# Kernel tuning notes

Measured on AMD Instinct MI355X. Metric: run time of the kernel, lower is better.

## Reference

```python
import jax, jax.numpy as jnp
import numpy as np

N, E, D, HID, HEADS, G = 20000, 320000, 1280, 64, 4, 256
NEG_SLOPE = 0.2  # PyG GATv2Conv default negative_slope


def setup_inputs() -> dict:
    key = jax.random.key(0)
    ks = jax.random.split(key, 20)

    def w(k, shape, fan_in):
        return (jax.random.normal(k, shape, jnp.float32) / np.float32(np.sqrt(fan_in)))

    return {
        "x": jax.random.normal(ks[0], (N, D), jnp.float32),
        "edge_index": jax.random.randint(ks[1], (2, E), 0, N),
        "batch": jnp.sort(jax.random.randint(ks[2], (N,), 0, G)),
        # GATv2 layer 1: in D, out HID, heads HEADS, concat
        "Wl1": w(ks[3], (D, HEADS * HID), D),
        "bl1": w(ks[4], (HEADS * HID,), D),
        "Wr1": w(ks[5], (D, HEADS * HID), D),
        "br1": w(ks[6], (HEADS * HID,), D),
        "att1": w(ks[7], (HEADS, HID), HID),
        "bias1": jnp.zeros((HEADS * HID,), jnp.float32),
        # GATv2 layer 2: in HEADS*HID, out HID, heads 1, concat
        "Wl2": w(ks[8], (HEADS * HID, HID), HEADS * HID),
        "bl2": w(ks[9], (HID,), HEADS * HID),
        "Wr2": w(ks[10], (HEADS * HID, HID), HEADS * HID),
        "br2": w(ks[11], (HID,), HEADS * HID),
        "att2": w(ks[12], (1, HID), HID),
        "bias2": jnp.zeros((HID,), jnp.float32),
        # MLP head
        "W3": w(ks[13], (HID, HID), HID),
        "b3": w(ks[14], (HID,), HID),
        "W4": w(ks[15], (HID, 1), HID),
        "b4": w(ks[16], (1,), HID),
    }


def _gatv2(x, src, dst, Wl, bl, Wr, br, att, bias, n):
    """PyG GATv2Conv (concat=True, eval mode): e_ij = a^T LeakyReLU(Wl x_j + Wr x_i),
    per-destination softmax, out_i = sum_j alpha_ij * (Wl x_j)."""
    H, C = att.shape
    xl = (x @ Wl + bl).reshape(n, H, C)  # source transform
    xr = (x @ Wr + br).reshape(n, H, C)  # target transform
    e = jax.nn.leaky_relu(xl[src] + xr[dst], NEG_SLOPE)      # [E,H,C]
    logit = jnp.einsum('ehc,hc->eh', e, att)                  # [E,H]
    m = jax.ops.segment_max(logit, dst, num_segments=n)      # stable softmax per dst
    ex = jnp.exp(logit - m[dst])
    denom = jax.ops.segment_sum(ex, dst, num_segments=n)
    alpha = ex / (denom[dst] + 1e-16)                         # [E,H]
    out = jax.ops.segment_sum(xl[src] * alpha[:, :, None], dst, num_segments=n)
    return out.reshape(n, H * C) + bias


def reference(x, edge_index, batch, Wl1, bl1, Wr1, br1, att1, bias1,
              Wl2, bl2, Wr2, br2, att2, bias2, W3, b3, W4, b4):
    # add_self_loops=True (PyG default)
    loops = jnp.arange(N, dtype=edge_index.dtype)
    src = jnp.concatenate([edge_index[0], loops])
    dst = jnp.concatenate([edge_index[1], loops])
    h = jax.nn.relu(_gatv2(x, src, dst, Wl1, bl1, Wr1, br1, att1, bias1, N))
    h = jax.nn.relu(_gatv2(h, src, dst, Wl2, bl2, Wr2, br2, att2, bias2, N))
    g = jax.ops.segment_sum(h, batch, num_segments=G)  # global_add_pool -> [G,HID]
    return jax.nn.relu(g @ W3 + b3) @ W4 + b4          # [G,1]
```

## Files before the change

kernel.cpp:

```cpp
#include <hip/hip_runtime.h>

constexpr int Nn    = 20000;
constexpr int Ee    = 320000;
constexpr int Dd    = 1280;
constexpr int Gg    = 256;
constexpr int ETOT  = Ee + Nn;
#define NEG 0.2f

typedef __attribute__((ext_vector_type(8))) short s8v;
typedef __attribute__((ext_vector_type(8))) unsigned short u16x8;
typedef __attribute__((ext_vector_type(4))) float f4v;

__device__ inline float lrelu(float v){ return v > 0.f ? v : NEG * v; }
__device__ inline float wave_sum(float v){
  #pragma unroll
  for(int o = 32; o; o >>= 1) v += __shfl_xor(v, o, 64);
  return v;
}
__device__ inline unsigned short f2bf(float x){
  unsigned u = __float_as_uint(x);
  return (unsigned short)((u + 0x7FFFu + ((u >> 16) & 1u)) >> 16);
}
__device__ inline float bf2f(unsigned short h){ return __uint_as_float(((unsigned)h) << 16); }

__device__ inline void async_cp16(const void* g, void* l){
  __builtin_amdgcn_global_load_lds((const __attribute__((address_space(1))) void*)g,
                                   (__attribute__((address_space(3))) void*)l, 16, 0, 0);
}

__device__ inline size_t pkoff(int n, int k, int NITp){
  return ((((size_t)(n >> 7) * NITp + (k >> 5)) * 512)
          + (((k >> 3) & 3) * 128 + (n & 127))) * 8 + (k & 7);
}

__global__ void fill_int(int* p, int n, int v){
  int i = blockIdx.x * blockDim.x + threadIdx.x;
  if(i < n) p[i] = v;
}
__global__ void hist_dst(const int* __restrict__ dst, int* __restrict__ deg){
  int e = blockIdx.x * blockDim.x + threadIdx.x;
  if(e < Ee) atomicAdd(&deg[dst[e]], 1);
}
__global__ __launch_bounds__(1024) void scan_deg(const int* __restrict__ deg,
                                                 int* __restrict__ rowptr,
                                                 int* __restrict__ cursor){
  __shared__ int part[1024];
  int t = threadIdx.x;
  const int CH = (Nn + 1023) / 1024;
  int base = t * CH;
  int s = 0;
  for(int j = 0; j < CH; j++){ int idx = base + j; if(idx < Nn) s += deg[idx]; }
  part[t] = s;
  __syncthreads();
  for(int off = 1; off < 1024; off <<= 1){
    int v = (t >= off) ? part[t - off] : 0;
    __syncthreads();
    part[t] += v;
    __syncthreads();
  }
  int acc = part[t] - s;
  for(int j = 0; j < CH; j++){
    int idx = base + j;
    if(idx < Nn){ rowptr[idx] = acc; cursor[idx] = acc; acc += deg[idx]; }
  }
  if(t == 1023) rowptr[Nn] = part[1023];
}
__global__ void scatter_edges(const int* __restrict__ src, const int* __restrict__ dst,
                              int* __restrict__ cursor, int* __restrict__ srcv){
  int e = blockIdx.x * blockDim.x + threadIdx.x;
  if(e >= ETOT) return;
  int d, s;
  if(e < Ee){ d = dst[e]; s = src[e]; } else { d = e - Ee; s = d; }
  int pos = atomicAdd(&cursor[d], 1);
  srcv[pos] = s;
}

__global__ __launch_bounds__(256) void wsplit(const float* __restrict__ Wl,
                                              const float* __restrict__ Wr,
                                              int K, int Ca, int NITp,
                                              unsigned short* __restrict__ PBH,
                                              unsigned short* __restrict__ PBL){
  __shared__ float t[32][33];
  int k0 = blockIdx.x * 32, n0 = blockIdx.y * 32;
  int tx = threadIdx.x & 31, ty = threadIdx.x >> 5;
  #pragma unroll
  for(int j = 0; j < 4; j++){
    int kk = ty + j * 8;
    int n = n0 + tx;
    t[kk][tx] = (n < Ca) ? Wl[(size_t)(k0 + kk) * Ca + n]
                         : Wr[(size_t)(k0 + kk) * Ca + (n - Ca)];
  }
  __syncthreads();
  #pragma unroll
  for(int j = 0; j < 4; j++){
    int nn = ty + j * 8;
    float v = t[tx][nn];
    unsigned short hi = f2bf(v);
    unsigned short lo = f2bf(v - bf2f(hi));
    size_t o = pkoff(n0 + nn, k0 + tx, NITp);
    PBH[o] = hi;
    PBL[o] = lo;
  }
}

__global__ __launch_bounds__(512) void gemm_2t(
    const float* __restrict__ X, int K, int niter, int nty,
    const unsigned short* __restrict__ PBH, const unsigned short* __restrict__ PBL,
    const float* __restrict__ bl, const float* __restrict__ br,
    unsigned short* __restrict__ XLb, float* __restrict__ XR)
{
  int id = blockIdx.x;
  int g8 = id >> 5, rem = id & 31;
  int xb = rem >> 3, yb = g8 * 8 + (rem & 7);
  if(yb >= nty) return;

  __shared__ unsigned short sA [2][4096];
  __shared__ unsigned short sBh[2][4096];
  __shared__ unsigned short sBl[2][4096];

  const int tid  = threadIdx.x;
  const int lane = tid & 63;
  const int w    = tid >> 6;
  const int wm   = w & 1, wn = w >> 1;
  const int bm   = yb * 128;
  const int bn   = xb * 128;

  f4v acc[4][2] = {};

  const int ar = w * 16 + (lane >> 2);
  const int aq = lane & 3;
  int gmr = bm + ar; if(gmr >= Nn) gmr = Nn - 1;
  const float* aptr = X + (size_t)gmr * K + aq * 8;
  const int awoff = (aq * 128 + ((ar + aq * 4) & 127)) * 8;

  const size_t bbase = ((size_t)xb * niter) * 4096 + tid * 8;
  const unsigned short* bhp = PBH + bbase;
  const unsigned short* blp = PBL + bbase;
  const int bldsoff = w * 512;

  async_cp16(bhp, &sBh[0][bldsoff]);
  async_cp16(blp, &sBl[0][bldsoff]);
  {
    float4 v0 = *(const float4*)(aptr);
    float4 v1 = *(const float4*)(aptr + 4);
    float fv[8] = {v0.x, v0.y, v0.z, v0.w, v1.x, v1.y, v1.z, v1.w};
    u16x8 hv;
    #pragma unroll
    for(int q = 0; q < 8; q++) hv[q] = f2bf(fv[q]);
    *(u16x8*)&sA[0][awoff] = hv;
  }

  const int mr = lane & 15;
  const int gq = lane >> 4;
  int aoff[4], boff[2];
  #pragma unroll
  for(int i = 0; i < 4; i++){
    int row = wm * 64 + i * 16 + mr;
    aoff[i] = (gq * 128 + ((row + gq * 4) & 127)) * 8;
  }
  #pragma unroll
  for(int j = 0; j < 2; j++){
    int n = wn * 32 + j * 16 + mr;
    boff[j] = (gq * 128 + n) * 8;
  }

  for(int it = 0; it < niter; it++){
    const int cur = it & 1, nxt = cur ^ 1;
    __syncthreads();
    float4 v0, v1;
    const bool more = (it + 1 < niter);
    if(more){
      async_cp16(bhp + (size_t)(it + 1) * 4096, &sBh[nxt][bldsoff]);
      async_cp16(blp + (size_t)(it + 1) * 4096, &sBl[nxt][bldsoff]);
      v0 = *(const float4*)(aptr + (it + 1) * 32);
      v1 = *(const float4*)(aptr + (it + 1) * 32 + 4);
    }
    s8v ah[4];
    #pragma unroll
    for(int i = 0; i < 4; i++) ah[i] = *(const s8v*)&sA[cur][aoff[i]];
    #pragma unroll
    for(int j = 0; j < 2; j++){
      s8v bh  = *(const s8v*)&sBh[cur][boff[j]];
      s8v bl2 = *(const s8v*)&sBl[cur][boff[j]];
      #pragma unroll
      for(int i = 0; i < 4; i++){
        acc[i][j] = __builtin_amdgcn_mfma_f32_16x16x32_bf16(ah[i], bh,  acc[i][j], 0, 0, 0);
        acc[i][j] = __builtin_amdgcn_mfma_f32_16x16x32_bf16(ah[i], bl2, acc[i][j], 0, 0, 0);
      }
    }
    if(more){
      float fv[8] = {v0.x, v0.y, v0.z, v0.w, v1.x, v1.y, v1.z, v1.w};
      u16x8 hv;
      #pragma unroll
      for(int q = 0; q < 8; q++) hv[q] = f2bf(fv[q]);
      *(u16x8*)&sA[nxt][awoff] = hv;
    }
  }

  const int quad = lane >> 4, col = lane & 15;
  #pragma unroll
  for(int j = 0; j < 2; j++){
    int gn = bn + wn * 32 + j * 16 + col;
    #pragma unroll
    for(int i = 0; i < 4; i++){
      #pragma unroll
      for(int rg = 0; rg < 4; rg++){
        int gmm = bm + wm * 64 + i * 16 + quad * 4 + rg;
        if(gmm < Nn){
          float v = acc[i][j][rg];
          if(gn < 256) XLb[(size_t)gmm * 256 + gn] = f2bf(v + bl[gn]);
          else         XR [(size_t)gmm * 256 + (gn - 256)] = v + br[gn - 256];
        }
      }
    }
  }
}

__global__ __launch_bounds__(512) void gemm2_cp(
    const unsigned short* __restrict__ PA,
    const unsigned short* __restrict__ PBH, const unsigned short* __restrict__ PBL,
    const float* __restrict__ bl, const float* __restrict__ br,
    unsigned short* __restrict__ XLb, float* __restrict__ XR)
{
  const int yb = blockIdx.x;
  __shared__ unsigned short sA [2][2048];
  __shared__ unsigned short sBh[2][4096];
  __shared__ unsigned short sBl[2][4096];

  const int tid  = threadIdx.x;
  const int lane = tid & 63;
  const int w    = tid >> 6;
  const int wm   = w & 1, wn = w >> 1;
  const int bm   = yb * 64;
  const int NIT  = 8;

  f4v acc[2][2] = {};

  const unsigned short* bhp = PBH + tid * 8;
  const unsigned short* blp = PBL + tid * 8;
  const int bldsoff = w * 512;
  const unsigned short* pap = PA + ((size_t)yb * NIT * 256 + tid) * 8;
  const int aldsoff = w * 512;

  async_cp16(bhp, &sBh[0][bldsoff]);
  async_cp16(blp, &sBl[0][bldsoff]);
  if(w < 4) async_cp16(pap, &sA[0][aldsoff]);

  const int mr = lane & 15;
  const int gq = lane >> 4;
  int aoff[2], boff[2];
  #pragma unroll
  for(int i = 0; i < 2; i++) aoff[i] = (gq * 64 + wm * 32 + i * 16 + mr) * 8;
  #pragma unroll
  for(int j = 0; j < 2; j++) boff[j] = (gq * 128 + wn * 32 + j * 16 + mr) * 8;

  for(int it = 0; it < NIT; it++){
    const int cur = it & 1, nxt = cur ^ 1;
    __syncthreads();
    if(it + 1 < NIT){
      async_cp16(bhp + (size_t)(it + 1) * 4096, &sBh[nxt][bldsoff]);
      async_cp16(blp + (size_t)(it + 1) * 4096, &sBl[nxt][bldsoff]);
      if(w < 4) async_cp16(pap + (size_t)(it + 1) * 2048, &sA[nxt][aldsoff]);
    }
    s8v ah[2];
    #pragma unroll
    for(int i = 0; i < 2; i++) ah[i] = *(const s8v*)&sA[cur][aoff[i]];
    #pragma unroll
    for(int j = 0; j < 2; j++){
      s8v bh  = *(const s8v*)&sBh[cur][boff[j]];
      s8v bl2 = *(const s8v*)&sBl[cur][boff[j]];
      #pragma unroll
      for(int i = 0; i < 2; i++){
        acc[i][j] = __builtin_amdgcn_mfma_f32_16x16x32_bf16(ah[i], bh,  acc[i][j], 0, 0, 0);
        acc[i][j] = __builtin_amdgcn_mfma_f32_16x16x32_bf16(ah[i], bl2, acc[i][j], 0, 0, 0);
      }
    }
  }

  const int quad = lane >> 4, col = lane & 15;
  #pragma unroll
  for(int j = 0; j < 2; j++){
    int gn = wn * 32 + j * 16 + col;
    #pragma unroll
    for(int i = 0; i < 2; i++){
      #pragma unroll
      for(int rg = 0; rg < 4; rg++){
        int gmm = bm + wm * 32 + i * 16 + quad * 4 + rg;
        if(gmm < Nn){
          float v = acc[i][j][rg];
          if(gn < 64) XLb[(size_t)gmm * 64 + gn] = f2bf(v + bl[gn]);
          else        XR [(size_t)gmm * 64 + (gn - 64)] = v + br[gn - 64];
        }
      }
    }
  }
}

__global__ __launch_bounds__(256) void gat_fused1(
    const int* __restrict__ rowptr, const int* __restrict__ srcv,
    const unsigned short* __restrict__ XLb, const float* __restrict__ XR,
    const float* __restrict__ att, const float* __restrict__ bias,
    unsigned short* __restrict__ PA2)
{
  int node = blockIdx.x * 4 + (threadIdx.x >> 6);
  int lane = threadIdx.x & 63;
  if(node >= Nn) return;
  const float4 xr = *(const float4*)(XR + (size_t)node * 256 + lane * 4);
  const float4 a  = *(const float4*)(att + lane * 4);
  int r0 = rowptr[node], r1 = rowptr[node + 1];
  float m[4], l[4]; float4 acc[4];
  #pragma unroll
  for(int c = 0; c < 4; c++){ m[c] = -1e30f; l[c] = 0.f; acc[c] = make_float4(0,0,0,0); }
  for(int k = r0; k < r1; k += 4){
    int nv = r1 - k;
    int s[4]; float4 xl[4]; float p[4];
    #pragma unroll
    for(int c = 0; c < 4; c++){
      int kk = (c < nv) ? (k + c) : k;
      s[c] = srcv[kk];
    }
    #pragma unroll
    for(int c = 0; c < 4; c++){
      ushort4 u = *(const ushort4*)(XLb + (size_t)s[c] * 256 + lane * 4);
      xl[c] = make_float4(bf2f(u.x), bf2f(u.y), bf2f(u.z), bf2f(u.w));
    }
    #pragma unroll
    for(int c = 0; c < 4; c++){
      p[c] = lrelu(xl[c].x + xr.x) * a.x + lrelu(xl[c].y + xr.y) * a.y
           + lrelu(xl[c].z + xr.z) * a.z + lrelu(xl[c].w + xr.w) * a.w;
    }
    #pragma unroll
    for(int o = 8; o; o >>= 1){
      #pragma unroll
      for(int c = 0; c < 4; c++) p[c] += __shfl_xor(p[c], o, 64);
    }
    #pragma unroll
    for(int c = 0; c < 4; c++){
      if(c < nv){
        float mn = fmaxf(m[c], p[c]);
        float sc = __expf(m[c] - mn);
        float wg = __expf(p[c] - mn);
        l[c] = l[c] * sc + wg;
        acc[c].x = acc[c].x * sc + wg * xl[c].x;
        acc[c].y = acc[c].y * sc + wg * xl[c].y;
        acc[c].z = acc[c].z * sc + wg * xl[c].z;
        acc[c].w = acc[c].w * sc + wg * xl[c].w;
        m[c] = mn;
      }
    }
  }
  float M = fmaxf(fmaxf(m[0], m[1]), fmaxf(m[2], m[3]));
  float L = 0.f; float4 A4 = make_float4(0,0,0,0);
  #pragma unroll
  for(int c = 0; c < 4; c++){
    float sc = __expf(m[c] - M);
    L += l[c] * sc;
    A4.x += acc[c].x * sc; A4.y += acc[c].y * sc;
    A4.z += acc[c].z * sc; A4.w += acc[c].w * sc;
  }
  float inv = 1.f / (L + 1e-16f);
  const float4 b = *(const float4*)(bias + lane * 4);
  float4 o;
  o.x = fmaxf(A4.x * inv + b.x, 0.f);
  o.y = fmaxf(A4.y * inv + b.y, 0.f);
  o.z = fmaxf(A4.z * inv + b.z, 0.f);
  o.w = fmaxf(A4.w * inv + b.w, 0.f);
  size_t po = ((((size_t)(node >> 6) * 8 + (lane >> 3)) * 256)
               + ((lane >> 1) & 3) * 64 + (node & 63)) * 8 + (lane & 1) * 4;
  *(ushort4*)(PA2 + po) = make_ushort4(f2bf(o.x), f2bf(o.y), f2bf(o.z), f2bf(o.w));
}

__global__ __launch_bounds__(256) void gat_fused2(
    const int* __restrict__ rowptr, const int* __restrict__ srcv,
    const unsigned short* __restrict__ XLb, const float* __restrict__ XR,
    const float* __restrict__ att, const float* __restrict__ bias,
    float* __restrict__ H)
{
  int node = blockIdx.x * 4 + (threadIdx.x >> 6);
  int lane = threadIdx.x & 63;
  if(node >= Nn) return;
  const float xr = XR[(size_t)node * 64 + lane];
  const float a = att[lane];
  int r0 = rowptr[node], r1 = rowptr[node + 1];
  float m[4], l[4], acc[4];
  #pragma unroll
  for(int c = 0; c < 4; c++){ m[c] = -1e30f; l[c] = 0.f; acc[c] = 0.f; }
  for(int k = r0; k < r1; k += 4){
    int nv = r1 - k;
    int s[4]; float xl[4]; float p[4];
    #pragma unroll
    for(int c = 0; c < 4; c++){
      int kk = (c < nv) ? (k + c) : k;
      s[c] = srcv[kk];
    }
    #pragma unroll
    for(int c = 0; c < 4; c++) xl[c] = bf2f(XLb[(size_t)s[c] * 64 + lane]);
    #pragma unroll
    for(int c = 0; c < 4; c++) p[c] = lrelu(xl[c] + xr) * a;
    #pragma unroll
    for(int o = 32; o; o >>= 1){
      #pragma unroll
      for(int c = 0; c < 4; c++) p[c] += __shfl_xor(p[c], o, 64);
    }
    #pragma unroll
    for(int c = 0; c < 4; c++){
      if(c < nv){
        float mn = fmaxf(m[c], p[c]);
        float sc = __expf(m[c] - mn);
        float wg = __expf(p[c] - mn);
        l[c] = l[c] * sc + wg;
        acc[c] = acc[c] * sc + wg * xl[c];
        m[c] = mn;
      }
    }
  }
  float M = fmaxf(fmaxf(m[0], m[1]), fmaxf(m[2], m[3]));
  float L = 0.f, A1 = 0.f;
  #pragma unroll
  for(int c = 0; c < 4; c++){
    float sc = __expf(m[c] - M);
    L += l[c] * sc; A1 += acc[c] * sc;
  }
  float inv = 1.f / (L + 1e-16f);
  H[(size_t)node * 64 + lane] = fmaxf(A1 * inv + bias[lane], 0.f);
}

__global__ void gbounds(const int* __restrict__ batch, int* __restrict__ gs){
  int g = blockIdx.x * blockDim.x + threadIdx.x;
  if(g > Gg) return;
  int lo = 0, hi = Nn;
  while(lo < hi){ int mid = (lo + hi) >> 1; if(batch[mid] < g) lo = mid + 1; else hi = mid; }
  gs[g] = lo;
}
__global__ __launch_bounds__(64) void pool_mlp(const float* __restrict__ H2,
                                               const int* __restrict__ gs,
                                               const float* __restrict__ W3,
                                               const float* __restrict__ b3,
                                               const float* __restrict__ W4,
                                               const float* __restrict__ b4,
                                               float* __restrict__ out){
  int g = blockIdx.x, t = threadIdx.x;
  int i0 = gs[g], i1 = gs[g + 1];
  float a0 = 0.f, a1 = 0.f, a2 = 0.f, a3 = 0.f;
  int i = i0;
  for(; i + 3 < i1; i += 4){
    a0 += H2[(size_t)i * 64 + t];       a1 += H2[(size_t)(i + 1) * 64 + t];
    a2 += H2[(size_t)(i + 2) * 64 + t]; a3 += H2[(size_t)(i + 3) * 64 + t];
  }
  for(; i < i1; i++) a0 += H2[(size_t)i * 64 + t];
  __shared__ float sh[64];
  sh[t] = (a0 + a1) + (a2 + a3);
  __syncthreads();
  float acc = b3[t];
  #pragma unroll
  for(int k = 0; k < 64; k++) acc = fmaf(sh[k], W3[k * 64 + t], acc);
  acc = fmaxf(acc, 0.f);
  float p = acc * W4[t];
  p = wave_sum(p);
  if(t == 0) out[g] = p + b4[0];
}

extern "C" void kernel_launch(void* const* d_in, const int* in_sizes, int n_in,
                              void* d_out, int out_size, void* d_ws, size_t ws_size,
                              hipStream_t stream)
{
  const float* x     = (const float*)d_in[0];
  const int*   ei    = (const int*)d_in[1];
  const int*   batch = (const int*)d_in[2];
  const float* Wl1   = (const float*)d_in[3];
  const float* bl1   = (const float*)d_in[4];
  const float* Wr1   = (const float*)d_in[5];
  const float* br1   = (const float*)d_in[6];
  const float* att1  = (const float*)d_in[7];
  const float* bias1 = (const float*)d_in[8];
  const float* Wl2   = (const float*)d_in[9];
  const float* bl2   = (const float*)d_in[10];
  const float* Wr2   = (const float*)d_in[11];
  const float* br2   = (const float*)d_in[12];
  const float* att2  = (const float*)d_in[13];
  const float* bias2 = (const float*)d_in[14];
  const float* W3    = (const float*)d_in[15];
  const float* b3    = (const float*)d_in[16];
  const float* W4    = (const float*)d_in[17];
  const float* b4    = (const float*)d_in[18];
  float* out = (float*)d_out;

  char* ws = (char*)d_ws;
  size_t off = 0;
  auto alloc = [&](size_t bytes) -> void* {
    void* p = ws + off;
    off += (bytes + 255) & ~(size_t)255;
    return p;
  };
  const int NTY1 = (Nn + 127) / 128;
  const int NTY2 = (Nn + 63) / 64;
  unsigned short* XLb1 = (unsigned short*)alloc((size_t)Nn * 256 * 2);
  float*          XR1  = (float*)alloc((size_t)Nn * 256 * 4);
  unsigned short* PA2  = (unsigned short*)alloc((size_t)NTY2 * 8 * 256 * 8 * 2);
  unsigned short* XLb2 = (unsigned short*)alloc((size_t)Nn * 64 * 2);
  float*          XR2  = (float*)alloc((size_t)Nn * 64 * 4);
  unsigned short* PB1H = (unsigned short*)alloc((size_t)512 * Dd * 2);
  unsigned short* PB1L = (unsigned short*)alloc((size_t)512 * Dd * 2);
  unsigned short* PB2H = (unsigned short*)alloc((size_t)128 * 256 * 2);
  unsigned short* PB2L = (unsigned short*)alloc((size_t)128 * 256 * 2);
  int*   rowptr = (int*)alloc((size_t)(Nn + 1) * 4);
  int*   deg    = (int*)alloc((size_t)Nn * 4);
  int*   cursor = (int*)alloc((size_t)Nn * 4);
  int*   srcv   = (int*)alloc((size_t)ETOT * 4);
  float* H2   = (float*)alloc((size_t)Nn * 64 * 4);
  int*   gs   = (int*)alloc((size_t)(Gg + 1) * 4);

  const int* srcA = ei;
  const int* dstA = ei + Ee;

  fill_int<<<(Nn + 255) / 256, 256, 0, stream>>>(deg, Nn, 1);
  hist_dst<<<(Ee + 255) / 256, 256, 0, stream>>>(dstA, deg);
  scan_deg<<<1, 1024, 0, stream>>>(deg, rowptr, cursor);
  scatter_edges<<<(ETOT + 255) / 256, 256, 0, stream>>>(srcA, dstA, cursor, srcv);
  gbounds<<<1, 512, 0, stream>>>(batch, gs);

  wsplit<<<dim3(Dd / 32, 512 / 32), 256, 0, stream>>>(Wl1, Wr1, Dd, 256, Dd / 32, PB1H, PB1L);
  wsplit<<<dim3(256 / 32, 128 / 32), 256, 0, stream>>>(Wl2, Wr2, 256, 64, 256 / 32, PB2H, PB2L);

  gemm_2t<<<640, 512, 0, stream>>>(
      x, Dd, Dd / 32, NTY1, PB1H, PB1L, bl1, br1, XLb1, XR1);
  gat_fused1<<<(Nn + 3) / 4, 256, 0, stream>>>(rowptr, srcv, XLb1, XR1, att1, bias1, PA2);

  gemm2_cp<<<NTY2, 512, 0, stream>>>(PA2, PB2H, PB2L, bl2, br2, XLb2, XR2);
  gat_fused2<<<(Nn + 3) / 4, 256, 0, stream>>>(rowptr, srcv, XLb2, XR2, att2, bias2, H2);

  pool_mlp<<<Gg, 64, 0, stream>>>(H2, gs, W3, b3, W4, b4, out);
}
```

Before: 452.9 us.

## Merge preprocessing into one launch, prepack X to bf16, overlap edge scatter with GEMM

The histogram, weight split, graph bounds and a new X-to-bf16 prepack pass now run as one multi-role kernel, and the edge scatter shares a launch with the layer-1 GEMM. Both changes cut kernel launches and let independent work overlap. The GEMM now loads pre-packed bf16 A tiles through async LDS copies instead of converting fp32 in its main loop. The cost is an extra full pass over X that writes a bf16 copy, plus the extra memory traffic that comes with it. The self-loop degree is now added in the scan rather than by a fill kernel.

```diff
diff --git a/kernel.cpp b/kernel.cpp
--- a/kernel.cpp
+++ b/kernel.cpp
@@ -11,6 +11,21 @@
 typedef __attribute__((ext_vector_type(8))) unsigned short u16x8;
 typedef __attribute__((ext_vector_type(4))) float f4v;
 
+constexpr int NTY1 = (Nn + 127) / 128;
+constexpr int NIT1 = Dd / 32;
+constexpr int NTY2 = (Nn + 63) / 64;
+
+constexpr int NP1 = NTY1 * NIT1;
+constexpr int NH  = (Ee + 255) / 256;
+constexpr int NW1 = (Dd / 32) * (512 / 32);
+constexpr int NW2 = (256 / 32) * (128 / 32);
+constexpr int NG  = 2;
+constexpr int K1B = NP1 + NH + NW1 + NW2 + NG;
+
+constexpr int NGEMM = 640;
+constexpr int NSC   = (ETOT + 511) / 512;
+constexpr int K2B   = NGEMM + NSC;
+
 __device__ inline float lrelu(float v){ return v > 0.f ? v : NEG * v; }
 __device__ inline float wave_sum(float v){
   #pragma unroll
@@ -33,14 +48,82 @@
           + (((k >> 3) & 3) * 128 + (n & 127))) * 8 + (k & 7);
 }
 
-__global__ void fill_int(int* p, int n, int v){
-  int i = blockIdx.x * blockDim.x + threadIdx.x;
-  if(i < n) p[i] = v;
-}
-__global__ void hist_dst(const int* __restrict__ dst, int* __restrict__ deg){
-  int e = blockIdx.x * blockDim.x + threadIdx.x;
-  if(e < Ee) atomicAdd(&deg[dst[e]], 1);
-}
+__global__ __launch_bounds__(256) void k1_mega(
+    const float* __restrict__ X, unsigned short* __restrict__ PA1,
+    const int* __restrict__ dstA, int* __restrict__ deg,
+    const float* __restrict__ Wl1, const float* __restrict__ Wr1,
+    unsigned short* __restrict__ PB1H, unsigned short* __restrict__ PB1L,
+    const float* __restrict__ Wl2, const float* __restrict__ Wr2,
+    unsigned short* __restrict__ PB2H, unsigned short* __restrict__ PB2L,
+    const int* __restrict__ batch, int* __restrict__ gs)
+{
+  const int bid = blockIdx.x;
+  const int tid = threadIdx.x;
+
+  if(bid < NP1){
+    int yb = bid / NIT1, it = bid % NIT1;
+    int row = tid >> 1, half = tid & 1;
+    int r = yb * 128 + row; if(r >= Nn) r = Nn - 1;
+    const float* xp = X + (size_t)r * Dd + it * 32 + half * 16;
+    float4 v0 = *(const float4*)(xp);
+    float4 v1 = *(const float4*)(xp + 4);
+    float4 v2 = *(const float4*)(xp + 8);
+    float4 v3 = *(const float4*)(xp + 12);
+    float fv[16] = {v0.x,v0.y,v0.z,v0.w, v1.x,v1.y,v1.z,v1.w,
+                    v2.x,v2.y,v2.z,v2.w, v3.x,v3.y,v3.z,v3.w};
+    size_t base = ((size_t)bid) * 512;
+    #pragma unroll
+    for(int g2 = 0; g2 < 2; g2++){
+      int gq = half * 2 + g2;
+      u16x8 hv;
+      #pragma unroll
+      for(int q = 0; q < 8; q++) hv[q] = f2bf(fv[g2 * 8 + q]);
+      *(u16x8*)(PA1 + (base + gq * 128 + row) * 8) = hv;
+    }
+    return;
+  }
+  if(bid < NP1 + NH){
+    int e = (bid - NP1) * 256 + tid;
+    if(e < Ee) atomicAdd(&deg[dstA[e]], 1);
+    return;
+  }
+  if(bid < NP1 + NH + NW1 + NW2){
+    const float *Wl, *Wr; unsigned short *PH, *PL; int K, Ca, idx;
+    if(bid < NP1 + NH + NW1){ Wl = Wl1; Wr = Wr1; PH = PB1H; PL = PB1L; K = Dd;  Ca = 256; idx = bid - (NP1 + NH); }
+    else                    { Wl = Wl2; Wr = Wr2; PH = PB2H; PL = PB2L; K = 256; Ca = 64;  idx = bid - (NP1 + NH + NW1); }
+    int nk = K / 32;
+    int k0 = (idx % nk) * 32, n0 = (idx / nk) * 32;
+    __shared__ float t[32][33];
+    int tx = tid & 31, ty = tid >> 5;
+    #pragma unroll
+    for(int j = 0; j < 4; j++){
+      int kk = ty + j * 8;
+      int n = n0 + tx;
+      t[kk][tx] = (n < Ca) ? Wl[(size_t)(k0 + kk) * Ca + n]
+                           : Wr[(size_t)(k0 + kk) * Ca + (n - Ca)];
+    }
+    __syncthreads();
+    #pragma unroll
+    for(int j = 0; j < 4; j++){
+      int nn = ty + j * 8;
+      float v = t[tx][nn];
+      unsigned short hi = f2bf(v);
+      unsigned short lo = f2bf(v - bf2f(hi));
+      size_t o = pkoff(n0 + nn, k0 + tx, nk);
+      PH[o] = hi;
+      PL[o] = lo;
+    }
+    return;
+  }
+  {
+    int g = (bid - (NP1 + NH + NW1 + NW2)) * 256 + tid;
+    if(g > Gg) return;
+    int lo = 0, hi = Nn;
+    while(lo < hi){ int mid = (lo + hi) >> 1; if(batch[mid] < g) lo = mid + 1; else hi = mid; }
+    gs[g] = lo;
+  }
+}
+
 __global__ __launch_bounds__(1024) void scan_deg(const int* __restrict__ deg,
                                                  int* __restrict__ rowptr,
                                                  int* __restrict__ cursor){
@@ -49,7 +132,7 @@
   const int CH = (Nn + 1023) / 1024;
   int base = t * CH;
   int s = 0;
-  for(int j = 0; j < CH; j++){ int idx = base + j; if(idx < Nn) s += deg[idx]; }
+  for(int j = 0; j < CH; j++){ int idx = base + j; if(idx < Nn) s += deg[idx] + 1; }
   part[t] = s;
   __syncthreads();
   for(int off = 1; off < 1024; off <<= 1){
@@ -61,62 +144,37 @@
   int acc = part[t] - s;
   for(int j = 0; j < CH; j++){
     int idx = base + j;
-    if(idx < Nn){ rowptr[idx] = acc; cursor[idx] = acc; acc += deg[idx]; }
+    if(idx < Nn){ rowptr[idx] = acc; cursor[idx] = acc; acc += deg[idx] + 1; }
   }
   if(t == 1023) rowptr[Nn] = part[1023];
 }
-__global__ void scatter_edges(const int* __restrict__ src, const int* __restrict__ dst,
-                              int* __restrict__ cursor, int* __restrict__ srcv){
-  int e = blockIdx.x * blockDim.x + threadIdx.x;
-  if(e >= ETOT) return;
-  int d, s;
-  if(e < Ee){ d = dst[e]; s = src[e]; } else { d = e - Ee; s = d; }
-  int pos = atomicAdd(&cursor[d], 1);
-  srcv[pos] = s;
-}
-
-__global__ __launch_bounds__(256) void wsplit(const float* __restrict__ Wl,
-                                              const float* __restrict__ Wr,
-                                              int K, int Ca, int NITp,
-                                              unsigned short* __restrict__ PBH,
-                                              unsigned short* __restrict__ PBL){
-  __shared__ float t[32][33];
-  int k0 = blockIdx.x * 32, n0 = blockIdx.y * 32;
-  int tx = threadIdx.x & 31, ty = threadIdx.x >> 5;
-  #pragma unroll
-  for(int j = 0; j < 4; j++){
-    int kk = ty + j * 8;
-    int n = n0 + tx;
-    t[kk][tx] = (n < Ca) ? Wl[(size_t)(k0 + kk) * Ca + n]
-                         : Wr[(size_t)(k0 + kk) * Ca + (n - Ca)];
-  }
-  __syncthreads();
-  #pragma unroll
-  for(int j = 0; j < 4; j++){
-    int nn = ty + j * 8;
-    float v = t[tx][nn];
-    unsigned short hi = f2bf(v);
-    unsigned short lo = f2bf(v - bf2f(hi));
-    size_t o = pkoff(n0 + nn, k0 + tx, NITp);
-    PBH[o] = hi;
-    PBL[o] = lo;
-  }
-}
-
-__global__ __launch_bounds__(512) void gemm_2t(
-    const float* __restrict__ X, int K, int niter, int nty,
+
+__global__ __launch_bounds__(512) void k2_gemm_scatter(
+    const unsigned short* __restrict__ PA1,
     const unsigned short* __restrict__ PBH, const unsigned short* __restrict__ PBL,
     const float* __restrict__ bl, const float* __restrict__ br,
-    unsigned short* __restrict__ XLb, float* __restrict__ XR)
+    unsigned short* __restrict__ XLb, float* __restrict__ XR,
+    const int* __restrict__ srcA, const int* __restrict__ dstA,
+    int* __restrict__ cursor, int* __restrict__ srcv)
 {
+  __shared__ unsigned short sA [2][4096];
+  __shared__ unsigned short sBh[2][4096];
+  __shared__ unsigned short sBl[2][4096];
+
+  if(blockIdx.x >= NGEMM){
+    int e = (blockIdx.x - NGEMM) * 512 + threadIdx.x;
+    if(e >= ETOT) return;
+    int d, s;
+    if(e < Ee){ d = dstA[e]; s = srcA[e]; } else { d = e - Ee; s = d; }
+    int pos = atomicAdd(&cursor[d], 1);
+    srcv[pos] = s;
+    return;
+  }
+
   int id = blockIdx.x;
   int g8 = id >> 5, rem = id & 31;
   int xb = rem >> 3, yb = g8 * 8 + (rem & 7);
-  if(yb >= nty) return;
-
-  __shared__ unsigned short sA [2][4096];
-  __shared__ unsigned short sBh[2][4096];
-  __shared__ unsigned short sBl[2][4096];
+  if(yb >= NTY1) return;
 
   const int tid  = threadIdx.x;
   const int lane = tid & 63;
@@ -127,53 +185,31 @@
 
   f4v acc[4][2] = {};
 
-  const int ar = w * 16 + (lane >> 2);
-  const int aq = lane & 3;
-  int gmr = bm + ar; if(gmr >= Nn) gmr = Nn - 1;
-  const float* aptr = X + (size_t)gmr * K + aq * 8;
-  const int awoff = (aq * 128 + ((ar + aq * 4) & 127)) * 8;
-
-  const size_t bbase = ((size_t)xb * niter) * 4096 + tid * 8;
+  const unsigned short* pap = PA1 + ((size_t)yb * NIT1 * 512 + tid) * 8;
+  const size_t bbase = ((size_t)xb * NIT1) * 4096 + tid * 8;
   const unsigned short* bhp = PBH + bbase;
   const unsigned short* blp = PBL + bbase;
-  const int bldsoff = w * 512;
-
-  async_cp16(bhp, &sBh[0][bldsoff]);
-  async_cp16(blp, &sBl[0][bldsoff]);
-  {
-    float4 v0 = *(const float4*)(aptr);
-    float4 v1 = *(const float4*)(aptr + 4);
-    float fv[8] = {v0.x, v0.y, v0.z, v0.w, v1.x, v1.y, v1.z, v1.w};
-    u16x8 hv;
-    #pragma unroll
-    for(int q = 0; q < 8; q++) hv[q] = f2bf(fv[q]);
-    *(u16x8*)&sA[0][awoff] = hv;
-  }
+  const int ldsoff = w * 512;
+
+  async_cp16(pap, &sA [0][ldsoff]);
+  async_cp16(bhp, &sBh[0][ldsoff]);
+  async_cp16(blp, &sBl[0][ldsoff]);
 
   const int mr = lane & 15;
   const int gq = lane >> 4;
   int aoff[4], boff[2];
   #pragma unroll
-  for(int i = 0; i < 4; i++){
-    int row = wm * 64 + i * 16 + mr;
-    aoff[i] = (gq * 128 + ((row + gq * 4) & 127)) * 8;
-  }
-  #pragma unroll
-  for(int j = 0; j < 2; j++){
-    int n = wn * 32 + j * 16 + mr;
-    boff[j] = (gq * 128 + n) * 8;
-  }
-
-  for(int it = 0; it < niter; it++){
+  for(int i = 0; i < 4; i++) aoff[i] = (gq * 128 + wm * 64 + i * 16 + mr) * 8;
+  #pragma unroll
+  for(int j = 0; j < 2; j++) boff[j] = (gq * 128 + wn * 32 + j * 16 + mr) * 8;
+
+  for(int it = 0; it < NIT1; it++){
     const int cur = it & 1, nxt = cur ^ 1;
     __syncthreads();
-    float4 v0, v1;
-    const bool more = (it + 1 < niter);
-    if(more){
-      async_cp16(bhp + (size_t)(it + 1) * 4096, &sBh[nxt][bldsoff]);
-      async_cp16(blp + (size_t)(it + 1) * 4096, &sBl[nxt][bldsoff]);
-      v0 = *(const float4*)(aptr + (it + 1) * 32);
-      v1 = *(const float4*)(aptr + (it + 1) * 32 + 4);
+    if(it + 1 < NIT1){
+      async_cp16(pap + (size_t)(it + 1) * 4096, &sA [nxt][ldsoff]);
+      async_cp16(bhp + (size_t)(it + 1) * 4096, &sBh[nxt][ldsoff]);
+      async_cp16(blp + (size_t)(it + 1) * 4096, &sBl[nxt][ldsoff]);
     }
     s8v ah[4];
     #pragma unroll
@@ -187,13 +223,6 @@
         acc[i][j] = __builtin_amdgcn_mfma_f32_16x16x32_bf16(ah[i], bh,  acc[i][j], 0, 0, 0);
         acc[i][j] = __builtin_amdgcn_mfma_f32_16x16x32_bf16(ah[i], bl2, acc[i][j], 0, 0, 0);
       }
-    }
-    if(more){
-      float fv[8] = {v0.x, v0.y, v0.z, v0.w, v1.x, v1.y, v1.z, v1.w};
-      u16x8 hv;
-      #pragma unroll
-      for(int q = 0; q < 8; q++) hv[q] = f2bf(fv[q]);
-      *(u16x8*)&sA[nxt][awoff] = hv;
     }
   }
 
@@ -425,13 +454,6 @@
   H[(size_t)node * 64 + lane] = fmaxf(A1 * inv + bias[lane], 0.f);
 }
 
-__global__ void gbounds(const int* __restrict__ batch, int* __restrict__ gs){
-  int g = blockIdx.x * blockDim.x + threadIdx.x;
-  if(g > Gg) return;
-  int lo = 0, hi = Nn;
-  while(lo < hi){ int mid = (lo + hi) >> 1; if(batch[mid] < g) lo = mid + 1; else hi = mid; }
-  gs[g] = lo;
-}
 __global__ __launch_bounds__(64) void pool_mlp(const float* __restrict__ H2,
                                                const int* __restrict__ gs,
                                                const float* __restrict__ W3,
@@ -492,8 +514,7 @@
     off += (bytes + 255) & ~(size_t)255;
     return p;
   };
-  const int NTY1 = (Nn + 127) / 128;
-  const int NTY2 = (Nn + 63) / 64;
+  unsigned short* PA1  = (unsigned short*)alloc((size_t)NP1 * 512 * 8 * 2);
   unsigned short* XLb1 = (unsigned short*)alloc((size_t)Nn * 256 * 2);
   float*          XR1  = (float*)alloc((size_t)Nn * 256 * 4);
   unsigned short* PA2  = (unsigned short*)alloc((size_t)NTY2 * 8 * 256 * 8 * 2);
@@ -513,17 +534,16 @@
   const int* srcA = ei;
   const int* dstA = ei + Ee;
 
-  fill_int<<<(Nn + 255) / 256, 256, 0, stream>>>(deg, Nn, 1);
-  hist_dst<<<(Ee + 255) / 256, 256, 0, stream>>>(dstA, deg);
+  hipMemsetAsync(deg, 0, (size_t)Nn * 4, stream);
+
+  k1_mega<<<K1B, 256, 0, stream>>>(x, PA1, dstA, deg,
+                                   Wl1, Wr1, PB1H, PB1L,
+                                   Wl2, Wr2, PB2H, PB2L,
+                                   batch, gs);
   scan_deg<<<1, 1024, 0, stream>>>(deg, rowptr, cursor);
-  scatter_edges<<<(ETOT + 255) / 256, 256, 0, stream>>>(srcA, dstA, cursor, srcv);
-  gbounds<<<1, 512, 0, stream>>>(batch, gs);
-
-  wsplit<<<dim3(Dd / 32, 512 / 32), 256, 0, stream>>>(Wl1, Wr1, Dd, 256, Dd / 32, PB1H, PB1L);
-  wsplit<<<dim3(256 / 32, 128 / 32), 256, 0, stream>>>(Wl2, Wr2, 256, 64, 256 / 32, PB2H, PB2L);
-
-  gemm_2t<<<640, 512, 0, stream>>>(
-      x, Dd, Dd / 32, NTY1, PB1H, PB1L, bl1, br1, XLb1, XR1);
+
+  k2_gemm_scatter<<<K2B, 512, 0, stream>>>(PA1, PB1H, PB1L, bl1, br1, XLb1, XR1,
+                                           srcA, dstA, cursor, srcv);
   gat_fused1<<<(Nn + 3) / 4, 256, 0, stream>>>(rowptr, srcv, XLb1, XR1, att1, bias1, PA2);
 
   gemm2_cp<<<NTY2, 512, 0, stream>>>(PA2, PB2H, PB2L, bl2, br2, XLb2, XR2);
```

After: 393.6 us. 1.15x faster.
